# Optimization experiments

Measured on AMD Instinct MI355X. Metric: run time of the kernel, lower is better.

## Reference

```python
import jax, jax.numpy as jnp
import numpy as np

OUT_F = 11008
IN_F = 4096
BATCH = 4


def setup_inputs() -> dict:
    key = jax.random.key(0)
    k1, k2, k3, k4 = jax.random.split(key, 4)
    x = jax.random.normal(k1, (BATCH, IN_F), dtype=jnp.float32)
    # quantized int8 weight values live in [-127, 127]; stored as int32 here
    q_weight = jax.random.randint(k2, (OUT_F, IN_F), -127, 128, dtype=jnp.int32)
    # per-output-channel scales (positive, like abs_max / qmax)
    scales = jax.random.uniform(k3, (OUT_F,), dtype=jnp.float32, minval=0.001, maxval=0.05)
    bias = jax.random.normal(k4, (OUT_F,), dtype=jnp.float32)
    return {"x": x, "q_weight": q_weight, "scales": scales, "bias": bias}


def reference(x, q_weight, scales, bias):
    # dequantize: int8 weight * per-row scale -> fp32 weight [OUT_F, IN_F]
    dq_weight = q_weight.astype(jnp.float32) * scales[:, None]
    # F.linear: x @ W^T + b
    out = jnp.einsum("bi,oi->bo", x, dq_weight) + bias
    return out
```

## Files before the change

### kernel.cpp

```cpp
#include <hip/hip_runtime.h>

namespace {

constexpr int OUT_F = 11008;
constexpr int IN_F  = 4096;

typedef int   int4v   __attribute__((ext_vector_type(4)));
typedef float float4v __attribute__((ext_vector_type(4)));

constexpr int ROWS_PER_WAVE   = 2;
constexpr int WAVES_PER_BLOCK = 4;
constexpr int ROWS_PER_BLOCK  = ROWS_PER_WAVE * WAVES_PER_BLOCK;
constexpr int K_STEPS         = IN_F / (64 * 4);
constexpr int CHUNK           = 2;
constexpr int NCHUNK          = K_STEPS / CHUNK;
constexpr int DEPTH           = 3;

__global__ __launch_bounds__(256, 2) void qlinear_kernel(
    const float* __restrict__ x,
    const int*   __restrict__ qw,
    const float* __restrict__ scales,
    const float* __restrict__ bias,
    float*       __restrict__ out)
{
    __shared__ float4v xs[4 * (IN_F / 4)];

    const int tid = threadIdx.x;
    const float4v* xg = (const float4v*)x;
#pragma unroll
    for (int j = 0; j < (4 * IN_F / 4) / 256; ++j)
        xs[j * 256 + tid] = xg[j * 256 + tid];
    __syncthreads();

    const int lane = tid & 63;
    const int wid  = tid >> 6;
    const int row0 = blockIdx.x * ROWS_PER_BLOCK + wid * ROWS_PER_WAVE;

    const int4v* wp0 = (const int4v*)(qw + (size_t)row0 * IN_F);
    const int4v* wp1 = (const int4v*)(qw + (size_t)(row0 + 1) * IN_F);

    float acc[ROWS_PER_WAVE][4];
#pragma unroll
    for (int r = 0; r < ROWS_PER_WAVE; ++r)
#pragma unroll
        for (int b = 0; b < 4; ++b)
            acc[r][b] = 0.0f;

    int4v w[DEPTH][ROWS_PER_WAVE][CHUNK];

#pragma unroll
    for (int p = 0; p < DEPTH - 1; ++p) {
#pragma unroll
        for (int s = 0; s < CHUNK; ++s) {
            w[p][0][s] = wp0[(p * CHUNK + s) * 64 + lane];
            w[p][1][s] = wp1[(p * CHUNK + s) * 64 + lane];
        }
    }

#pragma unroll
    for (int c = 0; c < NCHUNK; ++c) {
        if (c + DEPTH - 1 < NCHUNK) {
            const int pf = (c + DEPTH - 1) % DEPTH;
#pragma unroll
            for (int s = 0; s < CHUNK; ++s) {
                w[pf][0][s] = wp0[((c + DEPTH - 1) * CHUNK + s) * 64 + lane];
                w[pf][1][s] = wp1[((c + DEPTH - 1) * CHUNK + s) * 64 + lane];
            }
        }

        const int cc = c % DEPTH;
#pragma unroll
        for (int s = 0; s < CHUNK; ++s) {
            const int k = c * CHUNK + s;
            float4v xv[4];
#pragma unroll
            for (int b = 0; b < 4; ++b)
                xv[b] = xs[b * (IN_F / 4) + k * 64 + lane];

#pragma unroll
            for (int r = 0; r < ROWS_PER_WAVE; ++r) {
                float4v wf;
                wf.x = (float)w[cc][r][s].x;
                wf.y = (float)w[cc][r][s].y;
                wf.z = (float)w[cc][r][s].z;
                wf.w = (float)w[cc][r][s].w;
#pragma unroll
                for (int b = 0; b < 4; ++b) {
                    acc[r][b] += wf.x * xv[b].x;
                    acc[r][b] += wf.y * xv[b].y;
                    acc[r][b] += wf.z * xv[b].z;
                    acc[r][b] += wf.w * xv[b].w;
                }
            }
        }
    }

#pragma unroll
    for (int r = 0; r < ROWS_PER_WAVE; ++r)
#pragma unroll
        for (int b = 0; b < 4; ++b) {
            float v = acc[r][b];
#pragma unroll
            for (int m = 32; m >= 1; m >>= 1)
                v += __shfl_xor(v, m, 64);
            acc[r][b] = v;
        }

    if (lane == 0) {
#pragma unroll
        for (int r = 0; r < ROWS_PER_WAVE; ++r) {
            const int row = row0 + r;
            const float s  = scales[row];
            const float bz = bias[row];
#pragma unroll
            for (int b = 0; b < 4; ++b)
                out[(size_t)b * OUT_F + row] = acc[r][b] * s + bz;
        }
    }
}

}

extern "C" void kernel_launch(void* const* d_in, const int* in_sizes, int n_in,
                              void* d_out, int out_size, void* d_ws, size_t ws_size,
                              hipStream_t stream) {
    const float* x      = (const float*)d_in[0];
    const int*   qw     = (const int*)d_in[1];
    const float* scales = (const float*)d_in[2];
    const float* bias   = (const float*)d_in[3];
    float*       out    = (float*)d_out;

    const int grid = OUT_F / ROWS_PER_BLOCK;
    qlinear_kernel<<<grid, 256, 0, stream>>>(x, qw, scales, bias, out);
}
```

Measured before the change: 34.61 us.

## Use persistent waves over row pairs with cross-pair weight prefetch

Result: slower. 136.8 us (+295.1%).

```diff
diff --git a/kernel.cpp b/kernel.cpp
--- a/kernel.cpp
+++ b/kernel.cpp
@@ -4,17 +4,17 @@
 
 constexpr int OUT_F = 11008;
 constexpr int IN_F  = 4096;
+constexpr int R4    = IN_F / 4;
+constexpr int NPAIR = OUT_F / 2;
+constexpr int NBLK  = 512;
+constexpr int NWAVE = NBLK * 4;
+constexpr int K_STEPS = IN_F / (64 * 4);
+constexpr int CHUNK  = 2;
+constexpr int NCHUNK = K_STEPS / CHUNK;
+constexpr int DEPTH  = 4;
 
 typedef int   int4v   __attribute__((ext_vector_type(4)));
 typedef float float4v __attribute__((ext_vector_type(4)));
-
-constexpr int ROWS_PER_WAVE   = 2;
-constexpr int WAVES_PER_BLOCK = 4;
-constexpr int ROWS_PER_BLOCK  = ROWS_PER_WAVE * WAVES_PER_BLOCK;
-constexpr int K_STEPS         = IN_F / (64 * 4);
-constexpr int CHUNK           = 2;
-constexpr int NCHUNK          = K_STEPS / CHUNK;
-constexpr int DEPTH           = 3;
 
 __global__ __launch_bounds__(256, 2) void qlinear_kernel(
     const float* __restrict__ x,
@@ -23,98 +23,118 @@
     const float* __restrict__ bias,
     float*       __restrict__ out)
 {
-    __shared__ float4v xs[4 * (IN_F / 4)];
+    __shared__ float4v xs[4 * R4];
 
-    const int tid = threadIdx.x;
+    const int tid  = threadIdx.x;
+    const int lane = tid & 63;
+    const int wid  = tid >> 6;
+    const int wave_gid = blockIdx.x * 4 + wid;
+
+    const int4v* qw4 = (const int4v*)qw;
+
+    int4v w[DEPTH][2][CHUNK];
+
+    const int p0 = wave_gid;
+    {
+        const int4v* a = qw4 + (size_t)(2 * p0) * R4;
+        const int4v* b = a + R4;
+#pragma unroll
+        for (int pc = 0; pc < DEPTH - 1; ++pc)
+#pragma unroll
+            for (int s = 0; s < CHUNK; ++s) {
+                w[pc][0][s] = a[(pc * CHUNK + s) * 64 + lane];
+                w[pc][1][s] = b[(pc * CHUNK + s) * 64 + lane];
+            }
+    }
+
     const float4v* xg = (const float4v*)x;
 #pragma unroll
-    for (int j = 0; j < (4 * IN_F / 4) / 256; ++j)
+    for (int j = 0; j < (4 * R4) / 256; ++j)
         xs[j * 256 + tid] = xg[j * 256 + tid];
     __syncthreads();
 
-    const int lane = tid & 63;
-    const int wid  = tid >> 6;
-    const int row0 = blockIdx.x * ROWS_PER_BLOCK + wid * ROWS_PER_WAVE;
+    for (int p = p0; p < NPAIR; p += NWAVE) {
+        const int4v* a = qw4 + (size_t)(2 * p) * R4;
+        const int4v* b = a + R4;
+        const int  pn       = p + NWAVE;
+        const bool has_next = pn < NPAIR;
+        const int4v* an = qw4 + (size_t)(2 * (has_next ? pn : p0)) * R4;
+        const int4v* bn = an + R4;
 
-    const int4v* wp0 = (const int4v*)(qw + (size_t)row0 * IN_F);
-    const int4v* wp1 = (const int4v*)(qw + (size_t)(row0 + 1) * IN_F);
-
-    float acc[ROWS_PER_WAVE][4];
+        float acc[2][4];
 #pragma unroll
-    for (int r = 0; r < ROWS_PER_WAVE; ++r)
+        for (int r = 0; r < 2; ++r)
 #pragma unroll
-        for (int b = 0; b < 4; ++b)
-            acc[r][b] = 0.0f;
-
-    int4v w[DEPTH][ROWS_PER_WAVE][CHUNK];
+            for (int bt = 0; bt < 4; ++bt)
+                acc[r][bt] = 0.0f;
 
 #pragma unroll
-    for (int p = 0; p < DEPTH - 1; ++p) {
+        for (int c = 0; c < NCHUNK; ++c) {
+            constexpr int D1 = DEPTH - 1;
+            const int vi = c + D1;
+            if (vi < NCHUNK) {
 #pragma unroll
-        for (int s = 0; s < CHUNK; ++s) {
-            w[p][0][s] = wp0[(p * CHUNK + s) * 64 + lane];
-            w[p][1][s] = wp1[(p * CHUNK + s) * 64 + lane];
-        }
-    }
+                for (int s = 0; s < CHUNK; ++s) {
+                    w[vi % DEPTH][0][s] = a[(vi * CHUNK + s) * 64 + lane];
+                    w[vi % DEPTH][1][s] = b[(vi * CHUNK + s) * 64 + lane];
+                }
+            } else if (has_next) {
+                const int vj = vi - NCHUNK;
+#pragma unroll
+                for (int s = 0; s < CHUNK; ++s) {
+                    w[vj % DEPTH][0][s] = an[(vj * CHUNK + s) * 64 + lane];
+                    w[vj % DEPTH][1][s] = bn[(vj * CHUNK + s) * 64 + lane];
+                }
+            }
+
+            const int cc = c % DEPTH;
+#pragma unroll
+            for (int s = 0; s < CHUNK; ++s) {
+                const int k = c * CHUNK + s;
+                float4v xv[4];
+#pragma unroll
+                for (int bt = 0; bt < 4; ++bt)
+                    xv[bt] = xs[bt * (R4 / 4) * 4 + k * 64 + lane];
 
 #pragma unroll
-    for (int c = 0; c < NCHUNK; ++c) {
-        if (c + DEPTH - 1 < NCHUNK) {
-            const int pf = (c + DEPTH - 1) % DEPTH;
+                for (int r = 0; r < 2; ++r) {
+                    float4v wf;
+                    wf.x = (float)w[cc][r][s].x;
+                    wf.y = (float)w[cc][r][s].y;
+                    wf.z = (float)w[cc][r][s].z;
+                    wf.w = (float)w[cc][r][s].w;
 #pragma unroll
-            for (int s = 0; s < CHUNK; ++s) {
-                w[pf][0][s] = wp0[((c + DEPTH - 1) * CHUNK + s) * 64 + lane];
-                w[pf][1][s] = wp1[((c + DEPTH - 1) * CHUNK + s) * 64 + lane];
+                    for (int bt = 0; bt < 4; ++bt) {
+                        acc[r][bt] += wf.x * xv[bt].x;
+                        acc[r][bt] += wf.y * xv[bt].y;
+                        acc[r][bt] += wf.z * xv[bt].z;
+                        acc[r][bt] += wf.w * xv[bt].w;
+                    }
+                }
             }
         }
 
-        const int cc = c % DEPTH;
 #pragma unroll
-        for (int s = 0; s < CHUNK; ++s) {
-            const int k = c * CHUNK + s;
-            float4v xv[4];
+        for (int r = 0; r < 2; ++r)
 #pragma unroll
-            for (int b = 0; b < 4; ++b)
-                xv[b] = xs[b * (IN_F / 4) + k * 64 + lane];
+            for (int bt = 0; bt < 4; ++bt) {
+                float v = acc[r][bt];
+#pragma unroll
+                for (int m = 32; m >= 1; m >>= 1)
+                    v += __shfl_xor(v, m, 64);
+                acc[r][bt] = v;
+            }
 
+        if (lane == 0) {
 #pragma unroll
-            for (int r = 0; r < ROWS_PER_WAVE; ++r) {
-                float4v wf;
-                wf.x = (float)w[cc][r][s].x;
-                wf.y = (float)w[cc][r][s].y;
-                wf.z = (float)w[cc][r][s].z;
-                wf.w = (float)w[cc][r][s].w;
+            for (int r = 0; r < 2; ++r) {
+                const int row = 2 * p + r;
+                const float sc = scales[row];
+                const float bz = bias[row];
 #pragma unroll
-                for (int b = 0; b < 4; ++b) {
-                    acc[r][b] += wf.x * xv[b].x;
-                    acc[r][b] += wf.y * xv[b].y;
-                    acc[r][b] += wf.z * xv[b].z;
-                    acc[r][b] += wf.w * xv[b].w;
-                }
+                for (int bt = 0; bt < 4; ++bt)
+                    out[(size_t)bt * OUT_F + row] = acc[r][bt] * sc + bz;
             }
-        }
-    }
-
-#pragma unroll
-    for (int r = 0; r < ROWS_PER_WAVE; ++r)
-#pragma unroll
-        for (int b = 0; b < 4; ++b) {
-            float v = acc[r][b];
-#pragma unroll
-            for (int m = 32; m >= 1; m >>= 1)
-                v += __shfl_xor(v, m, 64);
-            acc[r][b] = v;
-        }
-
-    if (lane == 0) {
-#pragma unroll
-        for (int r = 0; r < ROWS_PER_WAVE; ++r) {
-            const int row = row0 + r;
-            const float s  = scales[row];
-            const float bz = bias[row];
-#pragma unroll
-            for (int b = 0; b < 4; ++b)
-                out[(size_t)b * OUT_F + row] = acc[r][b] * s + bz;
         }
     }
 }
@@ -130,6 +150,5 @@
     const float* bias   = (const float*)d_in[3];
     float*       out    = (float*)d_out;
 
-    const int grid = OUT_F / ROWS_PER_BLOCK;
-    qlinear_kernel<<<grid, 256, 0, stream>>>(x, qw, scales, bias, out);
+    qlinear_kernel<<<NBLK, 256, 0, stream>>>(x, qw, scales, bias, out);
 }
```
